# Performance work log

Measured on AMD Instinct MI355X. Metric: run time of the kernel, lower is better.

## Reference

```python
import jax, jax.numpy as jnp
import numpy as np

EPS = 1e-5
K_GROUP = 8  # k_group_size


def setup_inputs() -> dict:
    key = jax.random.key(0)
    ks = jax.random.split(key, 8)
    C = 384  # encoder_channel
    rn = lambda k, s: (jax.random.normal(k, s, dtype=jnp.float32) * 0.05)
    return {
        "point_groups": jax.random.normal(ks[0], (4, 256, 32, 3), dtype=jnp.float32),
        # first_conv: Conv1d(3,128,1)+BN+ReLU+Conv1d(128,256,1)
        "W1": rn(ks[1], (128, 3)), "b1": jnp.zeros(128, jnp.float32),
        "gamma1": jnp.ones(128, jnp.float32), "beta1": jnp.zeros(128, jnp.float32),
        "W2": rn(ks[2], (256, 128)), "b2": jnp.zeros(256, jnp.float32),
        # second_conv: Conv1d(512,512,1)+BN+ReLU+Conv1d(512,C,1)
        "W3": rn(ks[3], (512, 512)), "b3": jnp.zeros(512, jnp.float32),
        "gamma3": jnp.ones(512, jnp.float32), "beta3": jnp.zeros(512, jnp.float32),
        "W4": rn(ks[4], (C, 512)), "b4": jnp.zeros(C, jnp.float32),
        # K_Norm affine (out_dim = C, matching declared parameter shapes)
        "alpha": jnp.ones((1, 1, 1, C), jnp.float32),
        "beta_aff": jnp.zeros((1, 1, 1, C), jnp.float32),
        # fusion_layer: Conv1d(2C,C,1)+BN+ReLU
        "Wf": rn(ks[5], (C, 2 * C)), "bf": jnp.zeros(C, jnp.float32),
        "gammaf": jnp.ones(C, jnp.float32), "betaf": jnp.zeros(C, jnp.float32),
    }


def _conv1x1(x, W, b):  # x: (B,Cin,L), W: (Cout,Cin)
    return jnp.einsum("bcl,oc->bol", x, W) + b[None, :, None]


def _bn(x, gamma, beta):  # training-mode BatchNorm1d over (batch, length)
    mu = jnp.mean(x, axis=(0, 2), keepdims=True)
    var = jnp.var(x, axis=(0, 2), keepdims=True)
    xh = (x - mu) * jax.lax.rsqrt(var + EPS)
    return xh * gamma[None, :, None] + beta[None, :, None]


def reference(point_groups, W1, b1, gamma1, beta1, W2, b2, W3, b3, gamma3, beta3,
              W4, b4, alpha, beta_aff, Wf, bf, gammaf, betaf):
    bs, g, n, _ = point_groups.shape
    C = W4.shape[0]
    pg = point_groups.reshape(bs * g, n, 3)  # (B', n, 3)

    # first_conv stack
    f = _conv1x1(pg.transpose(0, 2, 1), W1, b1)           # (B',128,n)
    f = jax.nn.relu(_bn(f, gamma1, beta1))
    f = _conv1x1(f, W2, b2)                               # (B',256,n)
    fg = jnp.max(f, axis=2, keepdims=True)                # (B',256,1)
    f = jnp.concatenate([jnp.broadcast_to(fg, f.shape), f], axis=1)  # (B',512,n)

    # second_conv stack
    f = _conv1x1(f, W3, b3)
    f = jax.nn.relu(_bn(f, gamma3, beta3))
    f = _conv1x1(f, W4, b4)                               # (B',C,n)
    feat = f.transpose(0, 2, 1)                           # (B',n,C)

    # KNN within each group (self included, as in KNN(xyz,xyz))
    sq = jnp.sum(pg * pg, axis=-1)                        # (B',n)
    d = sq[:, :, None] + sq[:, None, :] - 2.0 * jnp.einsum("bnc,bmc->bnm", pg, pg)
    _, idx = jax.lax.top_k(-d, K_GROUP)                   # (B',n,K)

    gather = jax.vmap(lambda a, i: a[i])
    knn_x = gather(feat, idx)                             # (B',n,K,C)

    # K_Norm: center-relative normalization by global scalar std (torch.std, ddof=1)
    mean_x = feat[:, :, None, :]
    dx = knn_x - mean_x
    std_x = jnp.std(dx, ddof=1)
    knn_x = dx / (std_x + EPS)
    knn_x = alpha * knn_x + beta_aff                      # (B',n,K,C)

    enhanced = jnp.mean(knn_x, axis=2)                    # mean over K -> (B',n,C)
    enhanced = jnp.mean(enhanced, axis=1)                 # pool over n -> (B',C)

    fg2 = jnp.max(f, axis=2)                              # (B',C)
    fused_in = jnp.concatenate([fg2, enhanced], axis=1)[:, :, None]  # (B',2C,1)
    fused = jax.nn.relu(_bn(_conv1x1(fused_in, Wf, bf), gammaf, betaf))[:, :, 0]
    return fused.reshape(bs, g, C)
```

## Files before the change

### kernel.cpp

```cpp
#include <hip/hip_runtime.h>
#include <math.h>

#define EPS 1e-5f

typedef __attribute__((ext_vector_type(8))) short s16x8;
typedef __attribute__((ext_vector_type(4))) float f32x4;

__device__ __forceinline__ unsigned short f2bf(float x) {
    unsigned u = __float_as_uint(x);
    u += 0x7fffu + ((u >> 16) & 1u);
    return (unsigned short)(u >> 16);
}
__device__ __forceinline__ float bf2f(unsigned short h) {
    return __uint_as_float(((unsigned)h) << 16);
}
__device__ __forceinline__ unsigned long long pack4bf(float a, float b, float c, float d) {
    return (unsigned long long)f2bf(a)
         | ((unsigned long long)f2bf(b) << 16)
         | ((unsigned long long)f2bf(c) << 32)
         | ((unsigned long long)f2bf(d) << 48);
}

template<int CTRL>
__device__ __forceinline__ float dppmov(float x) {
    return __int_as_float(__builtin_amdgcn_update_dpp(
        0, __float_as_int(x), CTRL, 0xF, 0xF, true));
}
__device__ __forceinline__ float red16_sum(float x) {
    x += dppmov<0xB1>(x);
    x += dppmov<0x4E>(x);
    x += dppmov<0x141>(x);
    x += dppmov<0x140>(x);
    return x;
}
__device__ __forceinline__ float red16_max(float x) {
    x = fmaxf(x, dppmov<0xB1>(x));
    x = fmaxf(x, dppmov<0x4E>(x));
    x = fmaxf(x, dppmov<0x141>(x));
    x = fmaxf(x, dppmov<0x140>(x));
    return x;
}

__global__ __launch_bounds__(128) void k1_conv1_knn(
    const float* __restrict__ pg, const float* __restrict__ W1,
    const float* __restrict__ b1,
    const float* __restrict__ W2, const float* __restrict__ W3,
    const float* __restrict__ W4, const float* __restrict__ Wf,
    unsigned short* __restrict__ h1b, float* __restrict__ p1s, float* __restrict__ p1q,
    int* __restrict__ idxw,
    unsigned short* __restrict__ W2b, unsigned short* __restrict__ W3b,
    unsigned short* __restrict__ W4b, unsigned short* __restrict__ Wfb)
{
    __shared__ float pgs[96];
    __shared__ float sqs[32];
    if (blockIdx.x >= 1024) {
        const int i = (blockIdx.x - 1024) * 128 + threadIdx.x;
        if (i < 32768)  W2b[i] = f2bf(W2[i]);
        if (i < 262144) W3b[i] = f2bf(W3[i]);
        if (i < 196608) W4b[i] = f2bf(W4[i]);
        if (i < 294912) Wfb[i] = f2bf(Wf[i]);
        return;
    }
    const int b = blockIdx.x;
    const int t = threadIdx.x;
    if (t < 96) pgs[t] = pg[b * 96 + t];
    __syncthreads();
    if (t < 32) {
        float x = pgs[t*3+0], y = pgs[t*3+1], z = pgs[t*3+2];
        sqs[t] = x*x + y*y + z*z;
    }
    __syncthreads();
    {
        const float w0 = W1[t*3+0], w1 = W1[t*3+1], w2 = W1[t*3+2];
        const float bb = b1[t];
        float s = 0.f, q = 0.f;
        unsigned short* hcol = h1b + (size_t)b*4096 + t;
        #pragma unroll
        for (int l = 0; l < 32; ++l) {
            float v = fmaf(w2, pgs[l*3+2], fmaf(w1, pgs[l*3+1], fmaf(w0, pgs[l*3+0], bb)));
            hcol[l*128] = f2bf(v); s += v; q += v*v;
        }
        p1s[b*128 + t] = s;
        p1q[b*128 + t] = q;
    }
    if (t < 32) {
        const float xl = pgs[t*3+0], yl = pgs[t*3+1], zl = pgs[t*3+2];
        const float sql = sqs[t];
        float dist[32];
        #pragma unroll
        for (int m = 0; m < 32; ++m) {
            float dot = xl*pgs[m*3+0] + yl*pgs[m*3+1] + zl*pgs[m*3+2];
            dist[m] = sql + sqs[m] - 2.f*dot;
        }
        unsigned used = 0u;
        int* orow = idxw + b*256 + t*8;
        #pragma unroll
        for (int j = 0; j < 8; ++j) {
            float best = 3.4e38f; int bi = 0;
            #pragma unroll
            for (int m = 0; m < 32; ++m) {
                if (!((used >> m) & 1u) && dist[m] < best) { best = dist[m]; bi = m; }
            }
            used |= (1u << bi);
            orow[j] = bi;
        }
    }
}

__global__ __launch_bounds__(256) void k_bn_fin2(
    const float* __restrict__ ps, const float* __restrict__ pq,
    int nPart, int nChan, float invN,
    const float* __restrict__ gamma, const float* __restrict__ beta,
    float* __restrict__ scale, float* __restrict__ shift)
{
    const int ob = blockIdx.x * 4;
    const int t = threadIdx.x;
    const int co = t & 3, i0 = t >> 2;
    float s = 0.f, q = 0.f;
    for (int i = i0; i < nPart; i += 64) {
        s += ps[(size_t)i*nChan + ob + co];
        q += pq[(size_t)i*nChan + ob + co];
    }
    #pragma unroll
    for (int off = 32; off >= 4; off >>= 1) {
        s += __shfl_down(s, off, 64);
        q += __shfl_down(q, off, 64);
    }
    __shared__ float ss[4][4], qs[4][4];
    const int wid = t >> 6, lane = t & 63;
    if (lane < 4) { ss[wid][lane] = s; qs[wid][lane] = q; }
    __syncthreads();
    if (t < 4) {
        float S = ss[0][t] + ss[1][t] + ss[2][t] + ss[3][t];
        float Q = qs[0][t] + qs[1][t] + qs[2][t] + qs[3][t];
        const int o = ob + t;
        float mu  = S * invN;
        float var = Q * invN - mu*mu;
        float sc  = gamma[o] * rsqrtf(var + EPS);
        scale[o] = sc;
        shift[o] = beta[o] - mu * sc;
    }
}

__global__ __launch_bounds__(512, 4) void k3_mfma(
    const unsigned short* __restrict__ h1b,
    const float* __restrict__ scale1, const float* __restrict__ shift1,
    const unsigned short* __restrict__ W2b, const float* __restrict__ b2,
    const unsigned short* __restrict__ W3b, const float* __restrict__ b3,
    unsigned short* __restrict__ h3b, float* __restrict__ p3s, float* __restrict__ p3q)
{
    const int g0 = blockIdx.x * 2;
    const int t = threadIdx.x;
    __shared__ __align__(16) unsigned short SB[17424];
    unsigned short* B1  = SB;
    unsigned short* F2  = SB;
    unsigned short* FGB = SB + 16896;

    {
        const int l = t >> 3, c0 = (t & 7) * 16;
        const int g = g0 + (l >> 5);
        #pragma unroll
        for (int h = 0; h < 2; ++h) {
            s16x8 hv = *(const s16x8*)(h1b + (size_t)g*4096 + (l & 31)*128 + c0 + h*8);
            unsigned short ov[8];
            #pragma unroll
            for (int e = 0; e < 8; ++e) {
                int c = c0 + h*8 + e;
                float v = fmaxf(fmaf(bf2f((unsigned short)hv[e]), scale1[c], shift1[c]), 0.f);
                ov[e] = f2bf(v);
            }
            uint4 o4;
            o4.x = (unsigned)ov[0] | ((unsigned)ov[1] << 16);
            o4.y = (unsigned)ov[2] | ((unsigned)ov[3] << 16);
            o4.z = (unsigned)ov[4] | ((unsigned)ov[5] << 16);
            o4.w = (unsigned)ov[6] | ((unsigned)ov[7] << 16);
            *(uint4*)&B1[l*136 + c0 + h*8] = o4;
        }
    }
    __syncthreads();

    const int wave = t >> 6;
    const int lane = t & 63;
    const int m    = lane & 15;
    const int quad = lane >> 4;

    f32x4 acc2[2][4];
    #pragma unroll
    for (int mt = 0; mt < 2; ++mt)
        #pragma unroll
        for (int n = 0; n < 4; ++n)
            acc2[mt][n] = (f32x4){0.f, 0.f, 0.f, 0.f};

    #pragma unroll
    for (int kt = 0; kt < 4; ++kt) {
        s16x8 bv[4];
        #pragma unroll
        for (int nt = 0; nt < 4; ++nt)
            bv[nt] = *(const s16x8*)&B1[(nt*16 + m)*136 + kt*32 + quad*8];
        #pragma unroll
        for (int mt = 0; mt < 2; ++mt) {
            s16x8 av = *(const s16x8*)(W2b + (size_t)(wave*32 + mt*16 + m)*128 + kt*32 + quad*8);
            #pragma unroll
            for (int nt = 0; nt < 4; ++nt)
                acc2[mt][nt] = __builtin_amdgcn_mfma_f32_16x16x32_bf16(av, bv[nt], acc2[mt][nt], 0, 0, 0);
        }
    }
    __syncthreads();

    #pragma unroll
    for (int mt = 0; mt < 2; ++mt) {
        const int o0 = wave*32 + mt*16 + quad*4;
        #pragma unroll
        for (int r = 0; r < 4; ++r) {
            float bb = b2[o0 + r];
            #pragma unroll
            for (int nt = 0; nt < 4; ++nt) acc2[mt][nt][r] += bb;
        }
        #pragma unroll
        for (int nt = 0; nt < 4; ++nt) {
            const int row = nt*16 + m;
            *(unsigned long long*)&F2[row*264 + o0] =
                pack4bf(acc2[mt][nt][0], acc2[mt][nt][1], acc2[mt][nt][2], acc2[mt][nt][3]);
        }
        float f0[4], f1[4];
        #pragma unroll
        for (int r = 0; r < 4; ++r) {
            f0[r] = red16_max(fmaxf(acc2[mt][0][r], acc2[mt][1][r]));
            f1[r] = red16_max(fmaxf(acc2[mt][2][r], acc2[mt][3][r]));
        }
        if (m == 0) {
            *(unsigned long long*)&FGB[o0]       = pack4bf(f0[0], f0[1], f0[2], f0[3]);
            *(unsigned long long*)&FGB[264 + o0] = pack4bf(f1[0], f1[1], f1[2], f1[3]);
        }
    }
    __syncthreads();

    f32x4 facc[4];
    #pragma unroll
    for (int i = 0; i < 4; ++i) facc[i] = (f32x4){0.f, 0.f, 0.f, 0.f};
    #pragma unroll
    for (int kt = 0; kt < 8; ++kt) {
        s16x8 bg = *(const s16x8*)&FGB[(m & 1)*264 + kt*32 + quad*8];
        #pragma unroll
        for (int i = 0; i < 4; ++i) {
            s16x8 av = *(const s16x8*)(W3b + (size_t)((wave*4 + i)*16 + m)*512 + kt*32 + quad*8);
            facc[i] = __builtin_amdgcn_mfma_f32_16x16x32_bf16(av, bg, facc[i], 0, 0, 0);
        }
    }

    f32x4 acc3[4][4];
    #pragma unroll
    for (int mt = 0; mt < 4; ++mt) {
        #pragma unroll
        for (int r = 0; r < 4; ++r) {
            const int ob = (wave*4 + mt)*16 + quad*4 + r;
            float self = facc[mt][r];
            float oth  = dppmov<0xB1>(self);
            float fg_g0 = (m & 1) ? oth : self;
            float fg_g1 = (m & 1) ? self : oth;
            float bb = b3[ob];
            acc3[mt][0][r] = bb + fg_g0;
            acc3[mt][1][r] = bb + fg_g0;
            acc3[mt][2][r] = bb + fg_g1;
            acc3[mt][3][r] = bb + fg_g1;
        }
    }
    #pragma unroll 4
    for (int kt = 0; kt < 8; ++kt) {
        s16x8 bv[4];
        #pragma unroll
        for (int nt = 0; nt < 4; ++nt)
            bv[nt] = *(const s16x8*)&F2[(nt*16 + m)*264 + kt*32 + quad*8];
        #pragma unroll
        for (int mt = 0; mt < 4; ++mt) {
            s16x8 av = *(const s16x8*)(W3b + (size_t)((wave*4 + mt)*16 + m)*512 + 256 + kt*32 + quad*8);
            #pragma unroll
            for (int nt = 0; nt < 4; ++nt)
                acc3[mt][nt] = __builtin_amdgcn_mfma_f32_16x16x32_bf16(av, bv[nt], acc3[mt][nt], 0, 0, 0);
        }
    }

    unsigned short* dst = h3b + (size_t)blockIdx.x * 32768;
    #pragma unroll
    for (int mt = 0; mt < 4; ++mt) {
        const int ot = wave*4 + mt;
        const int o0 = ot*16 + quad*4;
        float s[4], q[4];
        #pragma unroll
        for (int r = 0; r < 4; ++r) {
            float x0 = acc3[mt][0][r], x1 = acc3[mt][1][r];
            float x2 = acc3[mt][2][r], x3 = acc3[mt][3][r];
            s[r] = (x0 + x1) + (x2 + x3);
            q[r] = (x0*x0 + x1*x1) + (x2*x2 + x3*x3);
        }
        {
            unsigned long long u0 = pack4bf(acc3[mt][0][0], acc3[mt][0][1], acc3[mt][0][2], acc3[mt][0][3]);
            unsigned long long u1 = pack4bf(acc3[mt][1][0], acc3[mt][1][1], acc3[mt][1][2], acc3[mt][1][3]);
            unsigned long long u2 = pack4bf(acc3[mt][2][0], acc3[mt][2][1], acc3[mt][2][2], acc3[mt][2][3]);
            unsigned long long u3 = pack4bf(acc3[mt][3][0], acc3[mt][3][1], acc3[mt][3][2], acc3[mt][3][3]);
            unsigned short* p = dst + (size_t)(ot*64 + lane) * 16;
            *(uint4*)(p)     = make_uint4((unsigned)u0, (unsigned)(u0 >> 32), (unsigned)u1, (unsigned)(u1 >> 32));
            *(uint4*)(p + 8) = make_uint4((unsigned)u2, (unsigned)(u2 >> 32), (unsigned)u3, (unsigned)(u3 >> 32));
        }
        #pragma unroll
        for (int r = 0; r < 4; ++r) {
            s[r] = red16_sum(s[r]);
            q[r] = red16_sum(q[r]);
        }
        if (m == 0) {
            #pragma unroll
            for (int r = 0; r < 4; ++r) {
                p3s[(size_t)blockIdx.x*512 + o0 + r] = s[r];
                p3q[(size_t)blockIdx.x*512 + o0 + r] = q[r];
            }
        }
    }
}

__global__ __launch_bounds__(512, 4) void k5_mfma(
    const unsigned short* __restrict__ h3b,
    const float* __restrict__ scale3, const float* __restrict__ shift3,
    const unsigned short* __restrict__ W4b, const float* __restrict__ b4,
    const int* __restrict__ idxw,
    float* __restrict__ fg2, float* __restrict__ A,
    float* __restrict__ S1p, float* __restrict__ S2p)
{
    const int g0 = blockIdx.x * 2;
    const int t = threadIdx.x;
    __shared__ __align__(16) unsigned short SB[33280];
    unsigned short* B4 = SB;
    unsigned short* XT = SB;
    unsigned short* Mm = SB + 30720;
    __shared__ int icnt[2][32];
    __shared__ float r1[2][8], r2[2][8];

    {
        const uint4* src = (const uint4*)(h3b + (size_t)blockIdx.x * 32768);
        for (int i = t; i < 4096; i += 512) {
            uint4 hv = src[i];
            const int flat16 = i >> 1, half = i & 1;
            const int ln = flat16 & 63, m2 = ln & 15, q2 = ln >> 4;
            const int wm = flat16 >> 6;
            const int o0 = wm*16 + q2*4;
            const float4 sc = *(const float4*)(scale3 + o0);
            const float4 sh = *(const float4*)(shift3 + o0);
            const int rowa = (half*2)*16 + m2;
            float a0 = fmaxf(fmaf(bf2f((unsigned short)(hv.x       )), sc.x, sh.x), 0.f);
            float a1 = fmaxf(fmaf(bf2f((unsigned short)(hv.x >> 16 )), sc.y, sh.y), 0.f);
            float a2 = fmaxf(fmaf(bf2f((unsigned short)(hv.y       )), sc.z, sh.z), 0.f);
            float a3 = fmaxf(fmaf(bf2f((unsigned short)(hv.y >> 16 )), sc.w, sh.w), 0.f);
            float b0 = fmaxf(fmaf(bf2f((unsigned short)(hv.z       )), sc.x, sh.x), 0.f);
            float b1 = fmaxf(fmaf(bf2f((unsigned short)(hv.z >> 16 )), sc.y, sh.y), 0.f);
            float b2 = fmaxf(fmaf(bf2f((unsigned short)(hv.w       )), sc.z, sh.z), 0.f);
            float b3 = fmaxf(fmaf(bf2f((unsigned short)(hv.w >> 16 )), sc.w, sh.w), 0.f);
            *(unsigned long long*)&B4[rowa*520 + o0]        = pack4bf(a0, a1, a2, a3);
            *(unsigned long long*)&B4[(rowa + 16)*520 + o0] = pack4bf(b0, b1, b2, b3);
        }
    }
    if (t < 64) icnt[t >> 5][t & 31] = 0;
    __syncthreads();

    const int wave = t >> 6;
    const int lane = t & 63;
    const int m    = lane & 15;
    const int quad = lane >> 4;

    f32x4 acc4[3][4];
    #pragma unroll
    for (int mt = 0; mt < 3; ++mt)
        #pragma unroll
        for (int n = 0; n < 4; ++n)
            acc4[mt][n] = (f32x4){0.f, 0.f, 0.f, 0.f};

    #pragma unroll 4
    for (int kt = 0; kt < 16; ++kt) {
        s16x8 bv[4];
        #pragma unroll
        for (int nt = 0; nt < 4; ++nt)
            bv[nt] = *(const s16x8*)&B4[(nt*16 + m)*520 + kt*32 + quad*8];
        #pragma unroll
        for (int mt = 0; mt < 3; ++mt) {
            s16x8 av = *(const s16x8*)(W4b + (size_t)(wave*48 + mt*16 + m)*512 + kt*32 + quad*8);
            #pragma unroll
            for (int nt = 0; nt < 4; ++nt)
                acc4[mt][nt] = __builtin_amdgcn_mfma_f32_16x16x32_bf16(av, bv[nt], acc4[mt][nt], 0, 0, 0);
        }
    }

    #pragma unroll
    for (int mt = 0; mt < 3; ++mt) {
        const int o0 = wave*48 + mt*16 + quad*4;
        float f0[4], f1[4];
        #pragma unroll
        for (int r = 0; r < 4; ++r) {
            float bb = b4[o0 + r];
            #pragma unroll
            for (int nt = 0; nt < 4; ++nt) acc4[mt][nt][r] += bb;
            f0[r] = red16_max(fmaxf(acc4[mt][0][r], acc4[mt][1][r]));
            f1[r] = red16_max(fmaxf(acc4[mt][2][r], acc4[mt][3][r]));
        }
        if (m == 0) {
            #pragma unroll
            for (int r = 0; r < 4; ++r) {
                fg2[(size_t)g0*384 + o0 + r]     = f0[r];
                fg2[(size_t)(g0+1)*384 + o0 + r] = f1[r];
            }
        }
    }
    __syncthreads();

    #pragma unroll
    for (int mt = 0; mt < 3; ++mt) {
        const int o0 = wave*48 + mt*16 + quad*4;
        #pragma unroll
        for (int nt = 0; nt < 4; ++nt) {
            const int g = nt >> 1;
            const int l = (nt & 1)*16 + m;
            unsigned short* xg = XT + g*15360;
            #pragma unroll
            for (int r = 0; r < 4; ++r)
                xg[(o0 + r)*40 + l] = f2bf(acc4[mt][nt][r]);
        }
    }
    if (t < 64) {
        const int g = t >> 5, l = t & 31;
        uint4 z = make_uint4(0u, 0u, 0u, 0u);
        #pragma unroll
        for (int i = 0; i < 5; ++i)
            *(uint4*)&Mm[g*1280 + l*40 + i*8] = z;
    }
    __syncthreads();

    if (t < 64) {
        const int g = t >> 5, l = t & 31;
        const int* ip = idxw + (size_t)(g0 + g)*256 + l*8;
        #pragma unroll
        for (int j = 0; j < 8; ++j) {
            int ix = ip[j];
            Mm[g*1280 + l*40 + ix] = 0x3F80;
            atomicAdd(&icnt[g][ix], 1);
        }
    }
    __syncthreads();

    float s1loc[2] = {0.f, 0.f}, s2loc[2] = {0.f, 0.f};
    #pragma unroll
    for (int g = 0; g < 2; ++g) {
        const float c0 = (float)icnt[g][m];
        const float c1 = (float)icnt[g][m + 16];
        const float w0 = c0 - 8.f, u0 = c0 + 8.f;
        const float w1 = c1 - 8.f, u1 = c1 + 8.f;
        #pragma unroll
        for (int mt = 0; mt < 3; ++mt) {
            const int o0 = wave*48 + mt*16 + quad*4;
            float Ap[4];
            #pragma unroll
            for (int r = 0; r < 4; ++r) {
                const float x0 = acc4[mt][g*2 + 0][r];
                const float x1 = acc4[mt][g*2 + 1][r];
                Ap[r] = w0*x0 + w1*x1;
                s1loc[g] += Ap[r];
                s2loc[g] += u0*x0*x0 + u1*x1*x1;
            }
            #pragma unroll
            for (int r = 0; r < 4; ++r)
                Ap[r] = red16_sum(Ap[r]);
            if (m == 0) {
                #pragma unroll
                for (int r = 0; r < 4; ++r)
                    A[(size_t)(g0 + g)*384 + o0 + r] = Ap[r];
            }
        }
    }

    #pragma unroll
    for (int g = 0; g < 2; ++g) {
        const unsigned short* xg = XT + g*15360;
        float cross = 0.f;
        #pragma unroll
        for (int lt = 0; lt < 2; ++lt) {
            s16x8 af = *(const s16x8*)&Mm[g*1280 + (lt*16 + m)*40 + quad*8];
            #pragma unroll
            for (int i = 0; i < 3; ++i) {
                const int oc = (wave*3 + i)*16 + m;
                s16x8 bfv = *(const s16x8*)&xg[oc*40 + quad*8];
                f32x4 sa = __builtin_amdgcn_mfma_f32_16x16x32_bf16(
                    af, bfv, (f32x4){0.f, 0.f, 0.f, 0.f}, 0, 0, 0);
                #pragma unroll
                for (int r = 0; r < 4; ++r) {
                    const int lp = lt*16 + quad*4 + r;
                    cross = fmaf(bf2f(xg[oc*40 + lp]), sa[r], cross);
                }
            }
        }
        s2loc[g] -= 2.f * cross;
    }

    #pragma unroll
    for (int g = 0; g < 2; ++g) {
        float sA = s1loc[g], sQ = s2loc[g];
        #pragma unroll
        for (int off = 32; off > 0; off >>= 1) {
            sA += __shfl_down(sA, off, 64);
            sQ += __shfl_down(sQ, off, 64);
        }
        if (lane == 0) { r1[g][wave] = sA; r2[g][wave] = sQ; }
    }
    __syncthreads();
    if (t < 2) {
        float S = 0.f, Q = 0.f;
        #pragma unroll
        for (int w = 0; w < 8; ++w) { S += r1[t][w]; Q += r2[t][w]; }
        S1p[g0 + t] = S;
        S2p[g0 + t] = Q;
    }
}

__global__ __launch_bounds__(384) void k7_fused(
    const float* __restrict__ fg2, const float* __restrict__ A,
    const float* __restrict__ alpha, const float* __restrict__ beta_aff,
    const float* __restrict__ S1p, const float* __restrict__ S2p,
    const unsigned short* __restrict__ Wfb, const float* __restrict__ bf,
    float* __restrict__ hf, float* __restrict__ pfs, float* __restrict__ pfq)
{
    const int blk    = blockIdx.x;
    const int slice  = blk >> 2;
    const int msplit = blk & 3;
    const int g0     = slice * 16;
    const int obase  = msplit * 96;
    const int t = threadIdx.x;
    __shared__ __align__(16) char smem[24832];
    unsigned short* xfb = (unsigned short*)smem;
    float* OTf = (float*)smem;
    __shared__ double rs[6], rq[6];
    __shared__ float stdsh;

    {
        double s = 0.0, q = 0.0;
        for (int i = t; i < 1024; i += 384) { s += (double)S1p[i]; q += (double)S2p[i]; }
        #pragma unroll
        for (int off = 32; off > 0; off >>= 1) {
            s += __shfl_down(s, off, 64);
            q += __shfl_down(q, off, 64);
        }
        if ((t & 63) == 0) { rs[t >> 6] = s; rq[t >> 6] = q; }
        __syncthreads();
        if (t == 0) {
            double S = 0.0, Q = 0.0;
            #pragma unroll
            for (int w = 0; w < 6; ++w) { S += rs[w]; Q += rq[w]; }
            const double N = 1024.0 * 32.0 * 8.0 * 384.0;
            double var = (Q - S*S/N) / (N - 1.0);
            stdsh = (float)sqrt(var);
        }
        __syncthreads();
    }
    const float inv = 1.f / (256.f * (stdsh + EPS));

    for (int i = t; i < 16*96; i += 384) {
        const int row = i / 96, c8 = (i % 96) * 8;
        const int g = g0 + row;
        float e[8];
        if (c8 < 384) {
            const float4* s0 = (const float4*)(fg2 + (size_t)g*384 + c8);
            float4 v0 = s0[0], v1 = s0[1];
            e[0]=v0.x; e[1]=v0.y; e[2]=v0.z; e[3]=v0.w;
            e[4]=v1.x; e[5]=v1.y; e[6]=v1.z; e[7]=v1.w;
        } else {
            const int cc = c8 - 384;
            const float4* s0 = (const float4*)(A + (size_t)g*384 + cc);
            float4 v0 = s0[0], v1 = s0[1];
            float av[8] = {v0.x,v0.y,v0.z,v0.w,v1.x,v1.y,v1.z,v1.w};
            #pragma unroll
            for (int j = 0; j < 8; ++j)
                e[j] = fmaf(alpha[cc+j] * inv, av[j], beta_aff[cc+j]);
        }
        uint4 o4;
        o4.x = (unsigned)f2bf(e[0]) | ((unsigned)f2bf(e[1]) << 16);
        o4.y = (unsigned)f2bf(e[2]) | ((unsigned)f2bf(e[3]) << 16);
        o4.z = (unsigned)f2bf(e[4]) | ((unsigned)f2bf(e[5]) << 16);
        o4.w = (unsigned)f2bf(e[6]) | ((unsigned)f2bf(e[7]) << 16);
        *(uint4*)&xfb[row*776 + c8] = o4;
    }
    __syncthreads();

    const int wave = t >> 6;
    const int lane = t & 63;
    const int m    = lane & 15;
    const int quad = lane >> 4;

    f32x4 acc = (f32x4){0.f, 0.f, 0.f, 0.f};
    #pragma unroll 4
    for (int kt = 0; kt < 24; ++kt) {
        s16x8 bv = *(const s16x8*)&xfb[m*776 + kt*32 + quad*8];
        s16x8 av = *(const s16x8*)(Wfb + (size_t)(obase + wave*16 + m)*768 + kt*32 + quad*8);
        acc = __builtin_amdgcn_mfma_f32_16x16x32_bf16(av, bv, acc, 0, 0, 0);
    }

    {
        const int o0 = obase + wave*16 + quad*4;
        float s[4], q[4];
        #pragma unroll
        for (int r = 0; r < 4; ++r) {
            acc[r] += bf[o0 + r];
            s[r] = red16_sum(acc[r]);
            q[r] = red16_sum(acc[r]*acc[r]);
        }
        if (m == 0) {
            #pragma unroll
            for (int r = 0; r < 4; ++r) {
                pfs[(size_t)slice*384 + o0 + r] = s[r];
                pfq[(size_t)slice*384 + o0 + r] = q[r];
            }
        }
    }
    __syncthreads();

    {
        const int lo0 = wave*16 + quad*4;
        #pragma unroll
        for (int r = 0; r < 4; ++r)
            OTf[m*100 + lo0 + r] = acc[r];
    }
    __syncthreads();

    {
        const int grp = t / 24, c4 = t % 24;
        float4 v = *(const float4*)&OTf[grp*100 + c4*4];
        *(float4*)(hf + (size_t)(g0 + grp)*384 + obase + c4*4) = v;
    }
}

__global__ __launch_bounds__(384) void k9_out(
    const float* __restrict__ hf,
    const float* __restrict__ pfs, const float* __restrict__ pfq,
    const float* __restrict__ gammaf, const float* __restrict__ betaf,
    float* __restrict__ out)
{
    const int blk = blockIdx.x, t = threadIdx.x;
    float S = 0.f, Q = 0.f;
    #pragma unroll 8
    for (int i = 0; i < 64; ++i) {
        S += pfs[(size_t)i*384 + t];
        Q += pfq[(size_t)i*384 + t];
    }
    const float mu  = S * (1.f/1024.f);
    const float var = Q * (1.f/1024.f) - mu*mu;
    const float sc  = gammaf[t] * rsqrtf(var + EPS);
    const float sh  = betaf[t] - mu * sc;
    const size_t base = (size_t)blk * 8 * 384;
    #pragma unroll
    for (int g = 0; g < 8; ++g) {
        float v = fmaf(hf[base + g*384 + t], sc, sh);
        out[base + g*384 + t] = fmaxf(v, 0.f);
    }
}

extern "C" void kernel_launch(void* const* d_in, const int* in_sizes, int n_in,
                              void* d_out, int out_size, void* d_ws, size_t ws_size,
                              hipStream_t stream) {
    const float* pg      = (const float*)d_in[0];
    const float* W1      = (const float*)d_in[1];
    const float* b1      = (const float*)d_in[2];
    const float* gamma1  = (const float*)d_in[3];
    const float* beta1   = (const float*)d_in[4];
    const float* W2      = (const float*)d_in[5];
    const float* b2      = (const float*)d_in[6];
    const float* W3      = (const float*)d_in[7];
    const float* b3      = (const float*)d_in[8];
    const float* gamma3  = (const float*)d_in[9];
    const float* beta3   = (const float*)d_in[10];
    const float* W4      = (const float*)d_in[11];
    const float* b4      = (const float*)d_in[12];
    const float* alpha   = (const float*)d_in[13];
    const float* beta_af = (const float*)d_in[14];
    const float* Wf      = (const float*)d_in[15];
    const float* bf      = (const float*)d_in[16];
    const float* gammaf  = (const float*)d_in[17];
    const float* betaf   = (const float*)d_in[18];
    float* out = (float*)d_out;

    float* w = (float*)d_ws;
    unsigned short* h1b = (unsigned short*)w; w += 1024*4096/2;
    unsigned short* h3b = (unsigned short*)w; w += 1024*16384/2;
    unsigned short* W2b = (unsigned short*)w; w += 32768/2;
    unsigned short* W3b = (unsigned short*)w; w += 262144/2;
    unsigned short* W4b = (unsigned short*)w; w += 196608/2;
    unsigned short* Wfb = (unsigned short*)w; w += 294912/2;
    float* hf     = w;  w += 1024*384;
    float* fg2    = w;  w += 1024*384;
    float* A      = w;  w += 1024*384;
    float* p1s    = w;  w += 1024*128;
    float* p1q    = w;  w += 1024*128;
    float* p3s    = w;  w += 1024*512;
    float* p3q    = w;  w += 1024*512;
    float* pfs    = w;  w += 64*384;
    float* pfq    = w;  w += 64*384;
    float* S1p    = w;  w += 1024;
    float* S2p    = w;  w += 1024;
    float* scale1 = w;  w += 128;
    float* shift1 = w;  w += 128;
    float* scale3 = w;  w += 512;
    float* shift3 = w;  w += 512;
    int*   idxw   = (int*)w;  w += 1024*256;

    hipLaunchKernelGGL(k1_conv1_knn, dim3(1024 + 2304), dim3(128), 0, stream,
                       pg, W1, b1, W2, W3, W4, Wf,
                       h1b, p1s, p1q, idxw, W2b, W3b, W4b, Wfb);
    hipLaunchKernelGGL(k_bn_fin2, dim3(32), dim3(256), 0, stream,
                       p1s, p1q, 1024, 128, 1.f/32768.f, gamma1, beta1, scale1, shift1);
    hipLaunchKernelGGL(k3_mfma, dim3(512), dim3(512), 0, stream,
                       h1b, scale1, shift1, W2b, b2, W3b, b3, h3b, p3s, p3q);
    hipLaunchKernelGGL(k_bn_fin2, dim3(128), dim3(256), 0, stream,
                       p3s, p3q, 512, 512, 1.f/32768.f, gamma3, beta3, scale3, shift3);
    hipLaunchKernelGGL(k5_mfma, dim3(512), dim3(512), 0, stream,
                       h3b, scale3, shift3, W4b, b4, idxw, fg2, A, S1p, S2p);
    hipLaunchKernelGGL(k7_fused, dim3(256), dim3(384), 0, stream,
                       fg2, A, alpha, beta_af, S1p, S2p, Wfb, bf, hf, pfs, pfq);
    hipLaunchKernelGGL(k9_out, dim3(128), dim3(384), 0, stream,
                       hf, pfs, pfq, gammaf, betaf, out);
}
```

Measured before the change: 205.3 us.

## Fuse conv3 and conv4 kernels via grid barriers, keeping activations in registers

Merges the W3 GEMM, its BatchNorm statistics finalization, and the W4 GEMM into one persistent kernel, using two atomic grid-wide barriers. The conv3 outputs stay in registers instead of being written to and re-read from a global bf16 buffer. Each block finalizes one channel's BN scale/shift from transposed partial sums. This removes the intermediate global traffic and two launches, but relies on all 512 blocks being co-resident and adds barrier spin latency and a memset.

```diff
diff --git a/kernel.cpp b/kernel.cpp
--- a/kernel.cpp
+++ b/kernel.cpp
@@ -39,6 +39,18 @@
     x = fmaxf(x, dppmov<0x141>(x));
     x = fmaxf(x, dppmov<0x140>(x));
     return x;
+}
+
+__device__ __forceinline__ void gbar(unsigned* __restrict__ bar, unsigned nblk) {
+    __threadfence();
+    __syncthreads();
+    if (threadIdx.x == 0) {
+        __hip_atomic_fetch_add(bar, 1u, __ATOMIC_ACQ_REL, __HIP_MEMORY_SCOPE_AGENT);
+        while (__hip_atomic_load(bar, __ATOMIC_ACQUIRE, __HIP_MEMORY_SCOPE_AGENT) < nblk)
+            __builtin_amdgcn_s_sleep(8);
+    }
+    __syncthreads();
+    __threadfence();
 }
 
 __global__ __launch_bounds__(128) void k1_conv1_knn(
@@ -142,19 +154,32 @@
     }
 }
 
-__global__ __launch_bounds__(512, 4) void k3_mfma(
+__global__ __launch_bounds__(512, 4) void k35_fused(
     const unsigned short* __restrict__ h1b,
     const float* __restrict__ scale1, const float* __restrict__ shift1,
     const unsigned short* __restrict__ W2b, const float* __restrict__ b2,
     const unsigned short* __restrict__ W3b, const float* __restrict__ b3,
-    unsigned short* __restrict__ h3b, float* __restrict__ p3s, float* __restrict__ p3q)
+    const float* __restrict__ gamma3, const float* __restrict__ beta3,
+    const unsigned short* __restrict__ W4b, const float* __restrict__ b4,
+    const int* __restrict__ idxw,
+    float* __restrict__ p3s, float* __restrict__ p3q,
+    float* __restrict__ scale3, float* __restrict__ shift3,
+    unsigned* __restrict__ barcnt,
+    float* __restrict__ fg2, float* __restrict__ A,
+    float* __restrict__ S1p, float* __restrict__ S2p)
 {
-    const int g0 = blockIdx.x * 2;
+    const int blk = blockIdx.x;
+    const int g0 = blk * 2;
     const int t = threadIdx.x;
-    __shared__ __align__(16) unsigned short SB[17424];
+    __shared__ __align__(16) unsigned short SB[33280];
     unsigned short* B1  = SB;
     unsigned short* F2  = SB;
     unsigned short* FGB = SB + 16896;
+    unsigned short* B4  = SB;
+    unsigned short* XT  = SB;
+    unsigned short* Mm  = SB + 30720;
+    __shared__ int icnt[2][32];
+    __shared__ float r1[2][8], r2[2][8];
 
     {
         const int l = t >> 3, c0 = (t & 7) * 16;
@@ -280,11 +305,9 @@
         }
     }
 
-    unsigned short* dst = h3b + (size_t)blockIdx.x * 32768;
     #pragma unroll
     for (int mt = 0; mt < 4; ++mt) {
-        const int ot = wave*4 + mt;
-        const int o0 = ot*16 + quad*4;
+        const int o0 = (wave*4 + mt)*16 + quad*4;
         float s[4], q[4];
         #pragma unroll
         for (int r = 0; r < 4; ++r) {
@@ -293,15 +316,6 @@
             s[r] = (x0 + x1) + (x2 + x3);
             q[r] = (x0*x0 + x1*x1) + (x2*x2 + x3*x3);
         }
-        {
-            unsigned long long u0 = pack4bf(acc3[mt][0][0], acc3[mt][0][1], acc3[mt][0][2], acc3[mt][0][3]);
-            unsigned long long u1 = pack4bf(acc3[mt][1][0], acc3[mt][1][1], acc3[mt][1][2], acc3[mt][1][3]);
-            unsigned long long u2 = pack4bf(acc3[mt][2][0], acc3[mt][2][1], acc3[mt][2][2], acc3[mt][2][3]);
-            unsigned long long u3 = pack4bf(acc3[mt][3][0], acc3[mt][3][1], acc3[mt][3][2], acc3[mt][3][3]);
-            unsigned short* p = dst + (size_t)(ot*64 + lane) * 16;
-            *(uint4*)(p)     = make_uint4((unsigned)u0, (unsigned)(u0 >> 32), (unsigned)u1, (unsigned)(u1 >> 32));
-            *(uint4*)(p + 8) = make_uint4((unsigned)u2, (unsigned)(u2 >> 32), (unsigned)u3, (unsigned)(u3 >> 32));
-        }
         #pragma unroll
         for (int r = 0; r < 4; ++r) {
             s[r] = red16_sum(s[r]);
@@ -310,60 +324,54 @@
         if (m == 0) {
             #pragma unroll
             for (int r = 0; r < 4; ++r) {
-                p3s[(size_t)blockIdx.x*512 + o0 + r] = s[r];
-                p3q[(size_t)blockIdx.x*512 + o0 + r] = q[r];
+                p3s[(size_t)(o0 + r)*512 + blk] = s[r];
+                p3q[(size_t)(o0 + r)*512 + blk] = q[r];
             }
         }
     }
-}
-
-__global__ __launch_bounds__(512, 4) void k5_mfma(
-    const unsigned short* __restrict__ h3b,
-    const float* __restrict__ scale3, const float* __restrict__ shift3,
-    const unsigned short* __restrict__ W4b, const float* __restrict__ b4,
-    const int* __restrict__ idxw,
-    float* __restrict__ fg2, float* __restrict__ A,
-    float* __restrict__ S1p, float* __restrict__ S2p)
-{
-    const int g0 = blockIdx.x * 2;
-    const int t = threadIdx.x;
-    __shared__ __align__(16) unsigned short SB[33280];
-    unsigned short* B4 = SB;
-    unsigned short* XT = SB;
-    unsigned short* Mm = SB + 30720;
-    __shared__ int icnt[2][32];
-    __shared__ float r1[2][8], r2[2][8];
+
+    gbar(&barcnt[0], 512u);
 
     {
-        const uint4* src = (const uint4*)(h3b + (size_t)blockIdx.x * 32768);
-        for (int i = t; i < 4096; i += 512) {
-            uint4 hv = src[i];
-            const int flat16 = i >> 1, half = i & 1;
-            const int ln = flat16 & 63, m2 = ln & 15, q2 = ln >> 4;
-            const int wm = flat16 >> 6;
-            const int o0 = wm*16 + q2*4;
-            const float4 sc = *(const float4*)(scale3 + o0);
-            const float4 sh = *(const float4*)(shift3 + o0);
-            const int rowa = (half*2)*16 + m2;
-            float a0 = fmaxf(fmaf(bf2f((unsigned short)(hv.x       )), sc.x, sh.x), 0.f);
-            float a1 = fmaxf(fmaf(bf2f((unsigned short)(hv.x >> 16 )), sc.y, sh.y), 0.f);
-            float a2 = fmaxf(fmaf(bf2f((unsigned short)(hv.y       )), sc.z, sh.z), 0.f);
-            float a3 = fmaxf(fmaf(bf2f((unsigned short)(hv.y >> 16 )), sc.w, sh.w), 0.f);
-            float b0 = fmaxf(fmaf(bf2f((unsigned short)(hv.z       )), sc.x, sh.x), 0.f);
-            float b1 = fmaxf(fmaf(bf2f((unsigned short)(hv.z >> 16 )), sc.y, sh.y), 0.f);
-            float b2 = fmaxf(fmaf(bf2f((unsigned short)(hv.w       )), sc.z, sh.z), 0.f);
-            float b3 = fmaxf(fmaf(bf2f((unsigned short)(hv.w >> 16 )), sc.w, sh.w), 0.f);
-            *(unsigned long long*)&B4[rowa*520 + o0]        = pack4bf(a0, a1, a2, a3);
-            *(unsigned long long*)&B4[(rowa + 16)*520 + o0] = pack4bf(b0, b1, b2, b3);
+        float vs = p3s[(size_t)blk*512 + t];
+        float vq = p3q[(size_t)blk*512 + t];
+        #pragma unroll
+        for (int off = 32; off > 0; off >>= 1) {
+            vs += __shfl_down(vs, off, 64);
+            vq += __shfl_down(vq, off, 64);
+        }
+        if (lane == 0) { r1[0][wave] = vs; r2[0][wave] = vq; }
+        __syncthreads();
+        if (t == 0) {
+            float S = 0.f, Q = 0.f;
+            #pragma unroll
+            for (int w = 0; w < 8; ++w) { S += r1[0][w]; Q += r2[0][w]; }
+            float mu  = S * (1.f/32768.f);
+            float var = Q * (1.f/32768.f) - mu*mu;
+            float sc  = gamma3[blk] * rsqrtf(var + EPS);
+            scale3[blk] = sc;
+            shift3[blk] = beta3[blk] - mu * sc;
+        }
+    }
+
+    gbar(&barcnt[1], 512u);
+
+    #pragma unroll
+    for (int mt = 0; mt < 4; ++mt) {
+        const int o0 = (wave*4 + mt)*16 + quad*4;
+        const float4 sc4 = *(const float4*)(scale3 + o0);
+        const float4 sh4 = *(const float4*)(shift3 + o0);
+        #pragma unroll
+        for (int nt = 0; nt < 4; ++nt) {
+            float v0 = fmaxf(fmaf(acc3[mt][nt][0], sc4.x, sh4.x), 0.f);
+            float v1 = fmaxf(fmaf(acc3[mt][nt][1], sc4.y, sh4.y), 0.f);
+            float v2 = fmaxf(fmaf(acc3[mt][nt][2], sc4.z, sh4.z), 0.f);
+            float v3 = fmaxf(fmaf(acc3[mt][nt][3], sc4.w, sh4.w), 0.f);
+            *(unsigned long long*)&B4[(nt*16 + m)*520 + o0] = pack4bf(v0, v1, v2, v3);
         }
     }
     if (t < 64) icnt[t >> 5][t & 31] = 0;
     __syncthreads();
-
-    const int wave = t >> 6;
-    const int lane = t & 63;
-    const int m    = lane & 15;
-    const int quad = lane >> 4;
 
     f32x4 acc4[3][4];
     #pragma unroll
@@ -703,18 +711,19 @@
     float* scale3 = w;  w += 512;
     float* shift3 = w;  w += 512;
     int*   idxw   = (int*)w;  w += 1024*256;
+    unsigned* barcnt = (unsigned*)w; w += 2;
+    (void)h3b;
 
     hipLaunchKernelGGL(k1_conv1_knn, dim3(1024 + 2304), dim3(128), 0, stream,
                        pg, W1, b1, W2, W3, W4, Wf,
                        h1b, p1s, p1q, idxw, W2b, W3b, W4b, Wfb);
     hipLaunchKernelGGL(k_bn_fin2, dim3(32), dim3(256), 0, stream,
                        p1s, p1q, 1024, 128, 1.f/32768.f, gamma1, beta1, scale1, shift1);
-    hipLaunchKernelGGL(k3_mfma, dim3(512), dim3(512), 0, stream,
-                       h1b, scale1, shift1, W2b, b2, W3b, b3, h3b, p3s, p3q);
-    hipLaunchKernelGGL(k_bn_fin2, dim3(128), dim3(256), 0, stream,
-                       p3s, p3q, 512, 512, 1.f/32768.f, gamma3, beta3, scale3, shift3);
-    hipLaunchKernelGGL(k5_mfma, dim3(512), dim3(512), 0, stream,
-                       h3b, scale3, shift3, W4b, b4, idxw, fg2, A, S1p, S2p);
+    hipMemsetAsync(barcnt, 0, 2 * sizeof(unsigned), stream);
+    hipLaunchKernelGGL(k35_fused, dim3(512), dim3(512), 0, stream,
+                       h1b, scale1, shift1, W2b, b2, W3b, b3, gamma3, beta3,
+                       W4b, b4, idxw, p3s, p3q, scale3, shift3, barcnt,
+                       fg2, A, S1p, S2p);
     hipLaunchKernelGGL(k7_fused, dim3(256), dim3(384), 0, stream,
                        fg2, A, alpha, beta_af, S1p, S2p, Wfb, bf, hf, pfs, pfq);
     hipLaunchKernelGGL(k9_out, dim3(128), dim3(384), 0, stream,
```

Result: slower. 591.9 us (+188.2%).
